# Optimization experiments

Hardware: AMD Instinct MI355X
Metric: run time of the kernel (lower is better)

## Reference

```python
import jax, jax.numpy as jnp
import numpy as np

N = 50000
E = 800000
D_IN = 128
D_H = 128
D_OUT = 128
G = 64
EPS = 1e-5


def setup_inputs() -> dict:
    key = jax.random.key(0)
    ks = jax.random.split(key, 16)
    s = 0.05
    x = jax.random.normal(ks[0], (N, D_IN), dtype=jnp.float32)
    edge_index = jax.random.randint(ks[1], (2, E), 0, N, dtype=jnp.int64)
    batch = jnp.sort(jax.random.randint(ks[2], (N,), 0, G, dtype=jnp.int64))
    return {
        "x": x,
        "edge_index": edge_index,
        "batch": batch,
        "W1": jax.random.normal(ks[3], (D_IN, D_H), jnp.float32) * s,
        "a_src1": jax.random.normal(ks[4], (D_H,), jnp.float32) * s,
        "a_dst1": jax.random.normal(ks[5], (D_H,), jnp.float32) * s,
        "b1": jnp.zeros((D_H,), jnp.float32),
        "W2": jax.random.normal(ks[6], (D_H, D_H), jnp.float32) * s,
        "a_src2": jax.random.normal(ks[7], (D_H,), jnp.float32) * s,
        "a_dst2": jax.random.normal(ks[8], (D_H,), jnp.float32) * s,
        "b2": jnp.zeros((D_H,), jnp.float32),
        "ln1_g": jnp.ones((D_H,), jnp.float32),
        "ln1_b": jnp.zeros((D_H,), jnp.float32),
        "ln2_g": jnp.ones((D_H,), jnp.float32),
        "ln2_b": jnp.zeros((D_H,), jnp.float32),
        "fc_W": jax.random.normal(ks[9], (D_H, D_OUT), jnp.float32) * s,
        "fc_b": jnp.zeros((D_OUT,), jnp.float32),
        "bn_g": jnp.ones((D_OUT,), jnp.float32),
        "bn_b": jnp.zeros((D_OUT,), jnp.float32),
    }


def gat_conv(x, src, dst, W, a_src, a_dst, b):
    # PyG GATConv, heads=1, concat=False. src=j (message source), dst=i (target).
    h = x @ W                              # [N, C]
    al_s = h @ a_src                       # [N]
    al_d = h @ a_dst                       # [N]
    alpha = jax.nn.leaky_relu(al_s[src] + al_d[dst], 0.2)  # [E']
    m = jax.ops.segment_max(alpha, dst, num_segments=N)    # segment softmax (stable)
    e = jnp.exp(alpha - m[dst])
    z = jax.ops.segment_sum(e, dst, num_segments=N)
    w = e / z[dst]                          # [E']
    out = jax.ops.segment_sum(w[:, None] * h[src], dst, num_segments=N)
    return out + b


def layer_norm(x, g, b):
    mu = jnp.mean(x, axis=-1, keepdims=True)
    var = jnp.mean((x - mu) ** 2, axis=-1, keepdims=True)
    return (x - mu) * jax.lax.rsqrt(var + EPS) * g + b


def reference(x, edge_index, batch, W1, a_src1, a_dst1, b1, W2, a_src2, a_dst2, b2,
              ln1_g, ln1_b, ln2_g, ln2_b, fc_W, fc_b, bn_g, bn_b):
    # add self loops (PyG GATConv default)
    sl = jnp.arange(N, dtype=edge_index.dtype)
    src = jnp.concatenate([edge_index[0], sl])
    dst = jnp.concatenate([edge_index[1], sl])

    h = jax.nn.relu(gat_conv(x, src, dst, W1, a_src1, a_dst1, b1))
    h = layer_norm(h, ln1_g, ln1_b)
    # dropout is identity in eval
    h = gat_conv(h, src, dst, W2, a_src2, a_dst2, b2)
    h = layer_norm(h, ln2_g, ln2_b)
    h = jax.nn.relu(h)

    # global mean pool over graphs
    sums = jax.ops.segment_sum(h, batch, num_segments=G)            # [G, D_H]
    cnts = jax.ops.segment_sum(jnp.ones((N,), h.dtype), batch, num_segments=G)
    pooled = sums / jnp.maximum(cnts, 1.0)[:, None]

    logits = pooled @ fc_W + fc_b                                   # [G, D_OUT]
    # BatchNorm1d (training-mode batch stats, biased variance)
    mu = jnp.mean(logits, axis=0)
    var = jnp.mean((logits - mu) ** 2, axis=0)
    logits = (logits - mu) * jax.lax.rsqrt(var + EPS) * bn_g + bn_b
    return logits
```

## Files before the change

kernel.cpp:

```cpp
#include <hip/hip_runtime.h>
#include <hip/hip_bf16.h>
#include <math.h>

#define N_NODES 50000
#define N_EDGES 800000
#define EN (N_EDGES + N_NODES)
#define D 128
#define G_GRAPHS 64
#define EPS 1e-5f
#define POOL_ROWS_PER_WAVE 64
#define N_TILES 3125
#define LIN_BLOCKS ((N_TILES + 15) / 16)

#define NBUCK 196
#define BCAP 6144
#define EPB 4096
#define BIN_BLOCKS ((EN + EPB - 1) / EPB)

typedef short short8 __attribute__((ext_vector_type(8)));
typedef float f32x4  __attribute__((ext_vector_type(4)));
typedef unsigned short us8 __attribute__((ext_vector_type(8)));

__device__ __forceinline__ float wave_reduce_sum(float v) {
  #pragma unroll
  for (int off = 32; off > 0; off >>= 1) v += __shfl_xor(v, off, 64);
  return v;
}
__device__ __forceinline__ int wave_reduce_sum_i(int v) {
  #pragma unroll
  for (int off = 32; off > 0; off >>= 1) v += __shfl_xor(v, off, 64);
  return v;
}

__device__ __forceinline__ float bf_to_f(unsigned short u) {
  union { unsigned int i; float f; } a;
  a.i = ((unsigned int)u) << 16;
  return a.f;
}
__device__ __forceinline__ unsigned short f_to_bf(float f) {
  union { float f; unsigned int i; } v; v.f = f;
  unsigned int r = v.i + 0x7FFF + ((v.i >> 16) & 1);
  return (unsigned short)(r >> 16);
}


__global__ __launch_bounds__(1024) void lin1_bin_kernel(
    const float* __restrict__ Xf, const float* __restrict__ W,
    const float* __restrict__ a_s, const float* __restrict__ a_d,
    unsigned short* __restrict__ Hb, float* __restrict__ AS, float* __restrict__ AD,
    const int* __restrict__ ei, int* __restrict__ gcnt, uint2* __restrict__ bedges) {
  int tid = threadIdx.x;
  if (blockIdx.x < BIN_BLOCKS) {
    __shared__ int hist[NBUCK], base[NBUCK], curl[NBUCK];
    for (int i = tid; i < NBUCK; i += 1024) { hist[i] = 0; curl[i] = 0; }
    __syncthreads();
    int e0 = blockIdx.x * EPB;
    int srcs[4], dsts[4];
    #pragma unroll
    for (int i = 0; i < 4; ++i) {
      int e = e0 + i * 1024 + tid;
      int s = -1, d = -1;
      if (e < N_EDGES)   { s = ei[e]; d = ei[N_EDGES + e]; }
      else if (e < EN)   { s = e - N_EDGES; d = s; }
      srcs[i] = s; dsts[i] = d;
      if (d >= 0) atomicAdd(&hist[d >> 8], 1);
    }
    __syncthreads();
    for (int i = tid; i < NBUCK; i += 1024)
      base[i] = atomicAdd(&gcnt[i], hist[i]);
    __syncthreads();
    #pragma unroll
    for (int i = 0; i < 4; ++i) {
      int d = dsts[i];
      if (d < 0) continue;
      int b = d >> 8;
      int pos = base[b] + atomicAdd(&curl[b], 1);
      if (pos < BCAP) bedges[(size_t)b * BCAP + pos] = make_uint2((unsigned)srcs[i], (unsigned)d);
    }
    return;
  }
  int bb = blockIdx.x - BIN_BLOCKS;
  __shared__ unsigned short Wl[D * D];
  #pragma unroll
  for (int it = 0; it < 16; ++it) {
    int flat = it * 1024 + tid;
    int r = flat >> 7, col = flat & 127;
    int c = r >> 5, rem = r & 31, quad = rem >> 3, j = rem & 7;
    int t = col >> 4, l = quad * 16 + (col & 15);
    Wl[((t * 4 + c) * 64 + l) * 8 + j] = f_to_bf(W[flat]);
  }
  int lane = tid & 63, wv = tid >> 6;
  int colI = lane & 15, quad = lane >> 4;
  float as_v[8], ad_v[8];
  #pragma unroll
  for (int t = 0; t < 8; ++t) { as_v[t] = a_s[t * 16 + colI]; ad_v[t] = a_d[t * 16 + colI]; }
  __syncthreads();
  int tile = bb * 16 + wv;
  if (tile < N_TILES) {
    int row0 = tile * 16;
    short8 afr[4];
    const float* xpf = Xf + (size_t)(row0 + colI) * D + quad * 8;
    #pragma unroll
    for (int c = 0; c < 4; ++c) {
      float4 f0 = *(const float4*)(xpf + c * 32);
      float4 f1 = *(const float4*)(xpf + c * 32 + 4);
      short8 a;
      a[0] = (short)f_to_bf(f0.x); a[1] = (short)f_to_bf(f0.y);
      a[2] = (short)f_to_bf(f0.z); a[3] = (short)f_to_bf(f0.w);
      a[4] = (short)f_to_bf(f1.x); a[5] = (short)f_to_bf(f1.y);
      a[6] = (short)f_to_bf(f1.z); a[7] = (short)f_to_bf(f1.w);
      afr[c] = a;
    }
    f32x4 acc[8];
    #pragma unroll
    for (int t = 0; t < 8; ++t) acc[t] = (f32x4){0.f, 0.f, 0.f, 0.f};
    #pragma unroll
    for (int t = 0; t < 8; ++t) {
      #pragma unroll
      for (int c = 0; c < 4; ++c) {
        short8 bfr = *(const short8*)&Wl[((t * 4 + c) * 64 + lane) * 8];
        acc[t] = __builtin_amdgcn_mfma_f32_16x16x32_bf16(afr[c], bfr, acc[t], 0, 0, 0);
      }
    }
    #pragma unroll
    for (int r = 0; r < 4; ++r) {
      int row = row0 + quad * 4 + r;
      float s = 0.f, dd = 0.f;
      #pragma unroll
      for (int t = 0; t < 8; ++t) {
        float v = acc[t][r];
        Hb[(size_t)row * D + t * 16 + colI] = f_to_bf(v);
        s  = fmaf(v, as_v[t], s);
        dd = fmaf(v, ad_v[t], dd);
      }
      #pragma unroll
      for (int off = 8; off >= 1; off >>= 1) {
        s  += __shfl_xor(s, off, 64);
        dd += __shfl_xor(dd, off, 64);
      }
      if (colI == 0) { AS[row] = s; AD[row] = dd; }
    }
  }
}

__global__ __launch_bounds__(256) void bucket_csr_kernel(
    const uint2* __restrict__ bedges, const int* __restrict__ gcnt,
    int* __restrict__ offs, int* __restrict__ esrc, float* __restrict__ sums) {
  __shared__ int hist[256], pex[256], curl[256], scanbuf[256];
  __shared__ int wsum[4];
  int b = blockIdx.x, t = threadIdx.x;
  if (b == 0) {
    for (int i = t; i < G_GRAPHS * D; i += 256) sums[i] = 0.f;
    if (t == 0) offs[N_NODES] = EN;
  }
  int pv = (t < b) ? gcnt[t] : 0;
  int v = wave_reduce_sum_i(pv);
  if ((t & 63) == 0) wsum[t >> 6] = v;
  hist[t] = 0; curl[t] = 0;
  __syncthreads();
  int gb = wsum[0] + wsum[1] + wsum[2] + wsum[3];
  int m = gcnt[b]; if (m > BCAP) m = BCAP;
  int node0 = b << 8;
  const uint2* be = bedges + (size_t)b * BCAP;
  for (int k = t; k < m; k += 256) atomicAdd(&hist[be[k].y & 255], 1);
  __syncthreads();
  int h = hist[t];
  scanbuf[t] = h;
  __syncthreads();
  #pragma unroll
  for (int off = 1; off < 256; off <<= 1) {
    int add = (t >= off) ? scanbuf[t - off] : 0;
    __syncthreads();
    scanbuf[t] += add;
    __syncthreads();
  }
  pex[t] = scanbuf[t] - h;
  int node = node0 + t;
  if (node < N_NODES) offs[node] = gb + pex[t];
  __syncthreads();
  for (int k = t; k < m; k += 256) {
    uint2 e = be[k];
    int n = e.y & 255;
    int r = atomicAdd(&curl[n], 1);
    esrc[gb + pex[n] + r] = (int)e.x;
  }
}


__global__ __launch_bounds__(1024) void linear_mfma_kernel(
    const unsigned short* __restrict__ Xb,
    const float* __restrict__ W,
    const float* __restrict__ a_s, const float* __restrict__ a_d,
    unsigned short* __restrict__ Hb, float* __restrict__ AS, float* __restrict__ AD) {
  __shared__ unsigned short Wl[D * D];
  int tid = threadIdx.x;
  #pragma unroll
  for (int it = 0; it < 16; ++it) {
    int flat = it * 1024 + tid;
    int r = flat >> 7, col = flat & 127;
    int c = r >> 5, rem = r & 31, quad = rem >> 3, j = rem & 7;
    int t = col >> 4, l = quad * 16 + (col & 15);
    Wl[((t * 4 + c) * 64 + l) * 8 + j] = f_to_bf(W[flat]);
  }
  int lane = tid & 63, wv = tid >> 6;
  int colI = lane & 15, quad = lane >> 4;
  float as_v[8], ad_v[8];
  #pragma unroll
  for (int t = 0; t < 8; ++t) { as_v[t] = a_s[t * 16 + colI]; ad_v[t] = a_d[t * 16 + colI]; }
  __syncthreads();
  int tile = blockIdx.x * 16 + wv;
  if (tile < N_TILES) {
    int row0 = tile * 16;
    short8 afr[4];
    const unsigned short* xp = Xb + (size_t)(row0 + colI) * D + quad * 8;
    #pragma unroll
    for (int c = 0; c < 4; ++c) afr[c] = *(const short8*)(xp + c * 32);
    f32x4 acc[8];
    #pragma unroll
    for (int t = 0; t < 8; ++t) acc[t] = (f32x4){0.f, 0.f, 0.f, 0.f};
    #pragma unroll
    for (int t = 0; t < 8; ++t) {
      #pragma unroll
      for (int c = 0; c < 4; ++c) {
        short8 bfr = *(const short8*)&Wl[((t * 4 + c) * 64 + lane) * 8];
        acc[t] = __builtin_amdgcn_mfma_f32_16x16x32_bf16(afr[c], bfr, acc[t], 0, 0, 0);
      }
    }
    #pragma unroll
    for (int r = 0; r < 4; ++r) {
      int row = row0 + quad * 4 + r;
      float s = 0.f, dd = 0.f;
      #pragma unroll
      for (int t = 0; t < 8; ++t) {
        float v = acc[t][r];
        Hb[(size_t)row * D + t * 16 + colI] = f_to_bf(v);
        s  = fmaf(v, as_v[t], s);
        dd = fmaf(v, ad_v[t], dd);
      }
      #pragma unroll
      for (int off = 8; off >= 1; off >>= 1) {
        s  += __shfl_xor(s, off, 64);
        dd += __shfl_xor(dd, off, 64);
      }
      if (colI == 0) { AS[row] = s; AD[row] = dd; }
    }
  }
}


__global__ __launch_bounds__(256, 4) void gat_kernel(
    const unsigned short* __restrict__ Hf, const float* __restrict__ AS,
    const float* __restrict__ AD,
    const int* __restrict__ offs, const int* __restrict__ esrc,
    const float* __restrict__ bias, const float* __restrict__ lng, const float* __restrict__ lnb,
    unsigned short* __restrict__ Out, int relu_after) {
  int tid = threadIdx.x;
  int lane = tid & 63;
  int wv = tid >> 6;
  int g4 = lane >> 4, mm = lane & 15;
  int node = blockIdx.x * 16 + wv * 4 + g4;
  if (node >= N_NODES) return;
  int beg = offs[node], end = offs[node + 1];
  float ald = AD[node];
  int base = lane & 48;
  float acc[8];
  #pragma unroll
  for (int d = 0; d < 8; ++d) acc[d] = 0.f;
  float zl = 0.f;
  const unsigned short* hq = Hf + 8 * mm;

  for (int c0 = beg; c0 < end; c0 += 16) {
    int nk = end - c0; if (nk > 16) nk = 16;
    int s_l = 0; float w_l = 0.f;
    if (mm < nk) {
      s_l = esrc[c0 + mm];
      float a = AS[s_l] + ald;
      a = (a > 0.f) ? a : 0.2f * a;
      w_l = __expf(a);
    }
    zl += w_l;
    int   sA = __shfl(s_l, base, 64),     sB = __shfl(s_l, base + 1, 64);
    int   sC = __shfl(s_l, base + 2, 64), sD = __shfl(s_l, base + 3, 64);
    float wA = __shfl(w_l, base, 64),     wB = __shfl(w_l, base + 1, 64);
    float wC = __shfl(w_l, base + 2, 64), wD = __shfl(w_l, base + 3, 64);
    us8 hA = *(const us8*)(hq + (unsigned)sA * D);
    us8 hB = *(const us8*)(hq + (unsigned)sB * D);
    us8 hC = *(const us8*)(hq + (unsigned)sC * D);
    us8 hD = *(const us8*)(hq + (unsigned)sD * D);
    for (int j = 4; j < nk; j += 4) {
      int   sA1 = __shfl(s_l, base + j, 64),     sB1 = __shfl(s_l, base + j + 1, 64);
      int   sC1 = __shfl(s_l, base + j + 2, 64), sD1 = __shfl(s_l, base + j + 3, 64);
      float wA1 = __shfl(w_l, base + j, 64),     wB1 = __shfl(w_l, base + j + 1, 64);
      float wC1 = __shfl(w_l, base + j + 2, 64), wD1 = __shfl(w_l, base + j + 3, 64);
      us8 hA1 = *(const us8*)(hq + (unsigned)sA1 * D);
      us8 hB1 = *(const us8*)(hq + (unsigned)sB1 * D);
      us8 hC1 = *(const us8*)(hq + (unsigned)sC1 * D);
      us8 hD1 = *(const us8*)(hq + (unsigned)sD1 * D);
      #pragma unroll
      for (int d = 0; d < 8; ++d) acc[d] = fmaf(wA, bf_to_f(hA[d]), acc[d]);
      #pragma unroll
      for (int d = 0; d < 8; ++d) acc[d] = fmaf(wB, bf_to_f(hB[d]), acc[d]);
      #pragma unroll
      for (int d = 0; d < 8; ++d) acc[d] = fmaf(wC, bf_to_f(hC[d]), acc[d]);
      #pragma unroll
      for (int d = 0; d < 8; ++d) acc[d] = fmaf(wD, bf_to_f(hD[d]), acc[d]);
      wA = wA1; wB = wB1; wC = wC1; wD = wD1;
      hA = hA1; hB = hB1; hC = hC1; hD = hD1;
    }
    #pragma unroll
    for (int d = 0; d < 8; ++d) acc[d] = fmaf(wA, bf_to_f(hA[d]), acc[d]);
    #pragma unroll
    for (int d = 0; d < 8; ++d) acc[d] = fmaf(wB, bf_to_f(hB[d]), acc[d]);
    #pragma unroll
    for (int d = 0; d < 8; ++d) acc[d] = fmaf(wC, bf_to_f(hC[d]), acc[d]);
    #pragma unroll
    for (int d = 0; d < 8; ++d) acc[d] = fmaf(wD, bf_to_f(hD[d]), acc[d]);
  }

  #pragma unroll
  for (int off = 8; off >= 1; off >>= 1) zl += __shfl_xor(zl, off, 64);
  float inv_z = 1.f / zl;
  const float4* bp = (const float4*)&bias[8 * mm];
  float4 bA4 = bp[0], bB4 = bp[1];
  float bb[8] = {bA4.x, bA4.y, bA4.z, bA4.w, bB4.x, bB4.y, bB4.z, bB4.w};
  float vv[8];
  #pragma unroll
  for (int d = 0; d < 8; ++d) {
    vv[d] = acc[d] * inv_z + bb[d];
    if (!relu_after) vv[d] = fmaxf(vv[d], 0.f);
  }
  float s8 = 0.f, ss = 0.f;
  #pragma unroll
  for (int d = 0; d < 8; ++d) { s8 += vv[d]; ss += vv[d] * vv[d]; }
  #pragma unroll
  for (int off = 8; off >= 1; off >>= 1) {
    s8 += __shfl_xor(s8, off, 64);
    ss += __shfl_xor(ss, off, 64);
  }
  float mean = s8 * (1.f / 128.f);
  float var = ss * (1.f / 128.f) - mean * mean;
  float inv = rsqrtf(var + EPS);
  const float4* gp = (const float4*)&lng[8 * mm];
  const float4* lp = (const float4*)&lnb[8 * mm];
  float4 gA = gp[0], gB = gp[1], lA = lp[0], lB = lp[1];
  float gg[8] = {gA.x, gA.y, gA.z, gA.w, gB.x, gB.y, gB.z, gB.w};
  float ll[8] = {lA.x, lA.y, lA.z, lA.w, lB.x, lB.y, lB.z, lB.w};
  us8 o;
  #pragma unroll
  for (int d = 0; d < 8; ++d) {
    float od = (vv[d] - mean) * inv * gg[d] + ll[d];
    if (relu_after) od = fmaxf(od, 0.f);
    o[d] = f_to_bf(od);
  }
  *(us8*)&Out[(size_t)node * D + 8 * mm] = o;
}


__global__ __launch_bounds__(256) void pool_sum_kernel(
    const unsigned short* __restrict__ Hf, const int* __restrict__ bat,
    float* __restrict__ sums) {
  int lane = threadIdx.x & 63;
  int g4 = lane >> 4, mm = lane & 15;
  int wv = blockIdx.x * 4 + (threadIdx.x >> 6);
  int r0 = wv * POOL_ROWS_PER_WAVE;
  if (r0 >= N_NODES) return;
  int r1 = r0 + POOL_ROWS_PER_WAVE;
  if (r1 > N_NODES) r1 = N_NODES;
  int rs = r0 + g4;
  if (rs >= r1) return;
  float acc[8];
  #pragma unroll
  for (int d = 0; d < 8; ++d) acc[d] = 0.f;
  int g = bat[rs];
  for (int r = rs; r < r1; r += 4) {
    int gr = bat[r];
    if (gr != g) {
      #pragma unroll
      for (int d = 0; d < 8; ++d) atomicAdd(&sums[g * D + 8 * mm + d], acc[d]);
      #pragma unroll
      for (int d = 0; d < 8; ++d) acc[d] = 0.f;
      g = gr;
    }
    us8 hv = *(const us8*)&Hf[(size_t)r * D + 8 * mm];
    #pragma unroll
    for (int d = 0; d < 8; ++d) acc[d] += bf_to_f(hv[d]);
  }
  #pragma unroll
  for (int d = 0; d < 8; ++d) atomicAdd(&sums[g * D + 8 * mm + d], acc[d]);
}

__device__ __forceinline__ int lower_bound_batch(const int* __restrict__ b, int val) {
  int lo = 0, hi = N_NODES;
  while (lo < hi) {
    int mid = (lo + hi) >> 1;
    if (b[mid] < val) lo = mid + 1; else hi = mid;
  }
  return lo;
}

__global__ void fc_kernel(const float* __restrict__ sums, const int* __restrict__ bat,
                          const float* __restrict__ fcW, const float* __restrict__ fcb,
                          float* __restrict__ logits) {
  int g = blockIdx.x;
  int d = threadIdx.x;
  int start = lower_bound_batch(bat, g);
  int end   = lower_bound_batch(bat, g + 1);
  float cnt = (float)(end - start);
  __shared__ float ps[D];
  ps[d] = sums[g * D + d] / fmaxf(cnt, 1.f);
  __syncthreads();
  float o = fcb[d];
  #pragma unroll 8
  for (int k = 0; k < D; ++k) o = fmaf(ps[k], fcW[k * D + d], o);
  logits[g * D + d] = o;
}

__global__ void bn_kernel(const float* __restrict__ logits, const float* __restrict__ g,
                          const float* __restrict__ b, float* __restrict__ out) {
  int d = threadIdx.x;
  float v[G_GRAPHS];
  float mu = 0.f;
  #pragma unroll
  for (int i = 0; i < G_GRAPHS; ++i) { v[i] = logits[i * D + d]; mu += v[i]; }
  mu *= (1.f / G_GRAPHS);
  float var = 0.f;
  #pragma unroll
  for (int i = 0; i < G_GRAPHS; ++i) { float t = v[i] - mu; var += t * t; }
  var *= (1.f / G_GRAPHS);
  float inv = rsqrtf(var + EPS);
  float gg = g[d], bb = b[d];
  #pragma unroll
  for (int i = 0; i < G_GRAPHS; ++i)
    out[i * D + d] = (v[i] - mu) * inv * gg + bb;
}


extern "C" void kernel_launch(void* const* d_in, const int* in_sizes, int n_in,
                              void* d_out, int out_size, void* d_ws, size_t ws_size,
                              hipStream_t stream) {
  const float* x    = (const float*)d_in[0];
  const int*   ei   = (const int*)d_in[1];
  const int*   bat  = (const int*)d_in[2];
  const float* W1   = (const float*)d_in[3];
  const float* as1  = (const float*)d_in[4];
  const float* ad1  = (const float*)d_in[5];
  const float* b1   = (const float*)d_in[6];
  const float* W2   = (const float*)d_in[7];
  const float* as2  = (const float*)d_in[8];
  const float* ad2  = (const float*)d_in[9];
  const float* b2   = (const float*)d_in[10];
  const float* ln1g = (const float*)d_in[11];
  const float* ln1b = (const float*)d_in[12];
  const float* ln2g = (const float*)d_in[13];
  const float* ln2b = (const float*)d_in[14];
  const float* fcW  = (const float*)d_in[15];
  const float* fcb  = (const float*)d_in[16];
  const float* bng  = (const float*)d_in[17];
  const float* bnb  = (const float*)d_in[18];

  char* p = (char*)d_ws;
  auto carve = [&](size_t bytes) { char* r = p; p += (bytes + 255) & ~(size_t)255; return r; };
  int*   offs  = (int*)carve((N_NODES + 1) * sizeof(int));
  int*   gcnt  = (int*)carve(NBUCK * sizeof(int));
  int*   esrc  = (int*)carve((size_t)EN * sizeof(int));
  float* AS    = (float*)carve(N_NODES * sizeof(float));
  float* AD    = (float*)carve(N_NODES * sizeof(float));
  float* LG    = (float*)carve((size_t)G_GRAPHS * D * sizeof(float));
  float* SUMS  = (float*)carve((size_t)G_GRAPHS * D * sizeof(float));
  unsigned short* B1b = (unsigned short*)carve((size_t)N_NODES * D * sizeof(unsigned short));
  unsigned short* B2b = (unsigned short*)carve((size_t)N_NODES * D * sizeof(unsigned short));
  uint2* bedges = (uint2*)B2b;

  const int RB = (N_NODES + 15) / 16;
  const int PB = (N_NODES + 4 * POOL_ROWS_PER_WAVE - 1) / (4 * POOL_ROWS_PER_WAVE);

  hipMemsetAsync(gcnt, 0, NBUCK * sizeof(int), stream);
  lin1_bin_kernel<<<BIN_BLOCKS + LIN_BLOCKS, 1024, 0, stream>>>(
      x, W1, as1, ad1, B1b, AS, AD, ei, gcnt, bedges);
  bucket_csr_kernel<<<NBUCK, 256, 0, stream>>>(bedges, gcnt, offs, esrc, SUMS);

  gat_kernel<<<RB, 256, 0, stream>>>(B1b, AS, AD, offs, esrc, b1, ln1g, ln1b, B2b, 0);
  linear_mfma_kernel<<<LIN_BLOCKS, 1024, 0, stream>>>(B2b, W2, as2, ad2, B1b, AS, AD);
  gat_kernel<<<RB, 256, 0, stream>>>(B1b, AS, AD, offs, esrc, b2, ln2g, ln2b, B2b, 1);

  pool_sum_kernel<<<PB, 256, 0, stream>>>(B2b, bat, SUMS);
  fc_kernel<<<G_GRAPHS, D, 0, stream>>>(SUMS, bat, fcW, fcb, LG);
  bn_kernel<<<1, D, 0, stream>>>(LG, bng, bnb, (float*)d_out);
}
```

Baseline: 240.8 us.

## Fuse global mean-pool summation into second GAT kernel via shared-memory partial sums

Removes the separate pool_sum kernel. The second GAT layer now accumulates its layer-normed, ReLU'd rows into per-block shared partial sums, split into two graph slots, and flushes them to global sums with atomics. This skips writing the final node features to memory and reading them back. The cost is shared-memory atomics in the epilogue and a block barrier. The per-node bounds check was removed, which is safe only because N is a multiple of 16. Blocks spanning more than two graphs would be wrong, though with 16 nodes per block and graph sizes near 780 this is unlikely.

```diff
diff --git a/kernel.cpp b/kernel.cpp
--- a/kernel.cpp
+++ b/kernel.cpp
@@ -8,7 +8,6 @@
 #define D 128
 #define G_GRAPHS 64
 #define EPS 1e-5f
-#define POOL_ROWS_PER_WAVE 64
 #define N_TILES 3125
 #define LIN_BLOCKS ((N_TILES + 15) / 16)
 
@@ -253,13 +252,18 @@
     const float* __restrict__ AD,
     const int* __restrict__ offs, const int* __restrict__ esrc,
     const float* __restrict__ bias, const float* __restrict__ lng, const float* __restrict__ lnb,
-    unsigned short* __restrict__ Out, int relu_after) {
+    unsigned short* __restrict__ Out, int relu_after,
+    const int* __restrict__ bat, float* __restrict__ sums, int pool) {
+  __shared__ float psum[2][D];
   int tid = threadIdx.x;
   int lane = tid & 63;
   int wv = tid >> 6;
   int g4 = lane >> 4, mm = lane & 15;
   int node = blockIdx.x * 16 + wv * 4 + g4;
-  if (node >= N_NODES) return;
+  if (pool) {
+    psum[tid >> 7][tid & 127] = 0.f;
+    __syncthreads();
+  }
   int beg = offs[node], end = offs[node + 1];
   float ald = AD[node];
   int base = lane & 48;
@@ -345,48 +349,33 @@
   float4 gA = gp[0], gB = gp[1], lA = lp[0], lB = lp[1];
   float gg[8] = {gA.x, gA.y, gA.z, gA.w, gB.x, gB.y, gB.z, gB.w};
   float ll[8] = {lA.x, lA.y, lA.z, lA.w, lB.x, lB.y, lB.z, lB.w};
-  us8 o;
-  #pragma unroll
-  for (int d = 0; d < 8; ++d) {
-    float od = (vv[d] - mean) * inv * gg[d] + ll[d];
-    if (relu_after) od = fmaxf(od, 0.f);
-    o[d] = f_to_bf(od);
-  }
-  *(us8*)&Out[(size_t)node * D + 8 * mm] = o;
-}
-
-
-__global__ __launch_bounds__(256) void pool_sum_kernel(
-    const unsigned short* __restrict__ Hf, const int* __restrict__ bat,
-    float* __restrict__ sums) {
-  int lane = threadIdx.x & 63;
-  int g4 = lane >> 4, mm = lane & 15;
-  int wv = blockIdx.x * 4 + (threadIdx.x >> 6);
-  int r0 = wv * POOL_ROWS_PER_WAVE;
-  if (r0 >= N_NODES) return;
-  int r1 = r0 + POOL_ROWS_PER_WAVE;
-  if (r1 > N_NODES) r1 = N_NODES;
-  int rs = r0 + g4;
-  if (rs >= r1) return;
-  float acc[8];
-  #pragma unroll
-  for (int d = 0; d < 8; ++d) acc[d] = 0.f;
-  int g = bat[rs];
-  for (int r = rs; r < r1; r += 4) {
-    int gr = bat[r];
-    if (gr != g) {
-      #pragma unroll
-      for (int d = 0; d < 8; ++d) atomicAdd(&sums[g * D + 8 * mm + d], acc[d]);
-      #pragma unroll
-      for (int d = 0; d < 8; ++d) acc[d] = 0.f;
-      g = gr;
-    }
-    us8 hv = *(const us8*)&Hf[(size_t)r * D + 8 * mm];
-    #pragma unroll
-    for (int d = 0; d < 8; ++d) acc[d] += bf_to_f(hv[d]);
-  }
-  #pragma unroll
-  for (int d = 0; d < 8; ++d) atomicAdd(&sums[g * D + 8 * mm + d], acc[d]);
+  if (!pool) {
+    us8 o;
+    #pragma unroll
+    for (int d = 0; d < 8; ++d) {
+      float od = (vv[d] - mean) * inv * gg[d] + ll[d];
+      if (relu_after) od = fmaxf(od, 0.f);
+      o[d] = f_to_bf(od);
+    }
+    *(us8*)&Out[(size_t)node * D + 8 * mm] = o;
+  } else {
+    int g  = bat[node];
+    int g0 = bat[blockIdx.x * 16];
+    int slot = (g != g0) ? 1 : 0;
+    #pragma unroll
+    for (int d = 0; d < 8; ++d) {
+      float od = (vv[d] - mean) * inv * gg[d] + ll[d];
+      if (relu_after) od = fmaxf(od, 0.f);
+      atomicAdd(&psum[slot][8 * mm + d], od);
+    }
+    __syncthreads();
+    if (tid < D) {
+      atomicAdd(&sums[g0 * D + tid], psum[0][tid]);
+    } else {
+      int g1 = bat[blockIdx.x * 16 + 15];
+      if (g1 != g0) atomicAdd(&sums[g1 * D + (tid - D)], psum[1][tid - D]);
+    }
+  }
 }
 
 __device__ __forceinline__ int lower_bound_batch(const int* __restrict__ b, int val) {
@@ -472,18 +461,18 @@
   uint2* bedges = (uint2*)B2b;
 
   const int RB = (N_NODES + 15) / 16;
-  const int PB = (N_NODES + 4 * POOL_ROWS_PER_WAVE - 1) / (4 * POOL_ROWS_PER_WAVE);
 
   hipMemsetAsync(gcnt, 0, NBUCK * sizeof(int), stream);
   lin1_bin_kernel<<<BIN_BLOCKS + LIN_BLOCKS, 1024, 0, stream>>>(
       x, W1, as1, ad1, B1b, AS, AD, ei, gcnt, bedges);
   bucket_csr_kernel<<<NBUCK, 256, 0, stream>>>(bedges, gcnt, offs, esrc, SUMS);
 
-  gat_kernel<<<RB, 256, 0, stream>>>(B1b, AS, AD, offs, esrc, b1, ln1g, ln1b, B2b, 0);
+  gat_kernel<<<RB, 256, 0, stream>>>(B1b, AS, AD, offs, esrc, b1, ln1g, ln1b, B2b, 0,
+                                     bat, SUMS, 0);
   linear_mfma_kernel<<<LIN_BLOCKS, 1024, 0, stream>>>(B2b, W2, as2, ad2, B1b, AS, AD);
-  gat_kernel<<<RB, 256, 0, stream>>>(B1b, AS, AD, offs, esrc, b2, ln2g, ln2b, B2b, 1);
-
-  pool_sum_kernel<<<PB, 256, 0, stream>>>(B2b, bat, SUMS);
+  gat_kernel<<<RB, 256, 0, stream>>>(B1b, AS, AD, offs, esrc, b2, ln2g, ln2b, B2b, 1,
+                                     bat, SUMS, 1);
+
   fc_kernel<<<G_GRAPHS, D, 0, stream>>>(SUMS, bat, fcW, fcb, LG);
   bn_kernel<<<1, D, 0, stream>>>(LG, bng, bnb, (float*)d_out);
 }
```

Result: slower. 247.2 us (+2.7%).
